# Performance work log

Measured on AMD Instinct MI355X. Metric: run time of the kernel, lower is better.

## Reference

```python
import jax, jax.numpy as jnp
import numpy as np

KS = 2            # kernel_size
NUM_SHARED = 3    # len(num_shared_channels)
NBR_PARAM = 3     # nbr_param_layers
COUT = 128        # num_shared_channels[-1] == num_inputs
NUM_INPUTS = 128
D_R = 320         # ts2vec_output_dims
GEN_LEN = NBR_PARAM * COUT * COUT * KS


def _causal_conv(x, w, b, d):
    # x: [N, Ci, T], w: [Co, Ci, K], b: [Co]; left-pad (K-1)*d == pad+chomp in torch
    N, Ci, T = x.shape
    K = w.shape[-1]
    pad = (K - 1) * d
    xp = jnp.pad(x, ((0, 0), (0, 0), (pad, 0)))
    out = jnp.zeros((N, w.shape[0], T), dtype=x.dtype)
    for k in range(K):  # K==2, tiny static loop
        out = out + jnp.einsum('oc,nct->not', w[:, :, k], xp[:, :, k * d:k * d + T])
    return out + b[None, :, None]


def _causal_conv_group(x, w, d):
    # groups=N conv with per-sample weights. x: [N, C, T], w: [N, Co, C, K], no bias
    N, C, T = x.shape
    K = w.shape[-1]
    pad = (K - 1) * d
    xp = jnp.pad(x, ((0, 0), (0, 0), (pad, 0)))
    out = jnp.zeros((N, w.shape[1], T), dtype=x.dtype)
    for k in range(K):
        out = out + jnp.einsum('noc,nct->not', w[..., k], xp[:, :, k * d:k * d + T])
    return out


def setup_inputs() -> dict:
    key = jax.random.key(0)
    ks = jax.random.split(key, 12)
    N, T = 16, 1024
    x = jax.random.normal(ks[0], (N, T, NUM_INPUTS), dtype=jnp.float32)
    r = jax.random.normal(ks[1], (N, D_R), dtype=jnp.float32)
    # shared TemporalBlock params (in==out==COUT, so no downsample conv)
    wscale = 1.0 / np.sqrt(COUT * KS)
    shared_w1 = wscale * jax.random.normal(ks[2], (NUM_SHARED, COUT, COUT, KS), dtype=jnp.float32)
    shared_b1 = 0.01 * jax.random.normal(ks[3], (NUM_SHARED, COUT), dtype=jnp.float32)
    shared_w2 = wscale * jax.random.normal(ks[4], (NUM_SHARED, COUT, COUT, KS), dtype=jnp.float32)
    shared_b2 = 0.01 * jax.random.normal(ks[5], (NUM_SHARED, COUT), dtype=jnp.float32)
    # hypernetwork (f_param_generator) + additive base weights (last_conv_layers)
    fparam_W = 0.01 * jax.random.normal(ks[6], (GEN_LEN, D_R), dtype=jnp.float32)
    fparam_b = 0.01 * jax.random.normal(ks[7], (GEN_LEN,), dtype=jnp.float32)
    last_bias = 0.001 * jax.random.normal(ks[8], (GEN_LEN,), dtype=jnp.float32) + 1.0 / (KS * COUT)
    # output head
    lin_W = (1.0 / np.sqrt(COUT)) * jax.random.normal(ks[9], (NUM_INPUTS, COUT), dtype=jnp.float32)
    lin_b = 0.01 * jax.random.normal(ks[10], (NUM_INPUTS,), dtype=jnp.float32)
    return {"x": x, "r": r, "f_out_same_in_size": 1,
            "shared_w1": shared_w1, "shared_b1": shared_b1,
            "shared_w2": shared_w2, "shared_b2": shared_b2,
            "fparam_W": fparam_W, "fparam_b": fparam_b, "last_bias": last_bias,
            "lin_W": lin_W, "lin_b": lin_b}


def reference(x, r, f_out_same_in_size, shared_w1, shared_b1, shared_w2, shared_b2,
              fparam_W, fparam_b, last_bias, lin_W, lin_b):
    N, T, _ = x.shape
    h = jnp.swapaxes(x, 1, 2)  # [N, C, T]
    # shared TemporalBlocks (dropout p=0 -> identity)
    for i in range(NUM_SHARED):
        d = 2 ** i
        res = h
        a = jax.nn.relu(_causal_conv(h, shared_w1[i], shared_b1[i], d))
        a = jax.nn.relu(_causal_conv(a, shared_w2[i], shared_b2[i], d))
        h = jax.nn.relu(a + res)
    # hypernet-generated per-sample grouped conv layers
    gen = r @ fparam_W.T + fparam_b + last_bias           # [N, GEN_LEN]
    allw = gen.reshape(NBR_PARAM, N, COUT, COUT, KS)      # same layout as torch .view
    for i in range(NBR_PARAM):
        d = 2 ** (NUM_SHARED + i)
        res = h
        c = _causal_conv_group(h, allw[i], d)
        h = jax.nn.relu(jax.nn.relu(c) + res)             # relu(dropout(relu(c)) + res), p=0
    out = jnp.einsum('nct,oc->nto', h, lin_W) + lin_b     # [N, T, NUM_INPUTS]
    if not f_out_same_in_size:
        out = out[:, -1, :]
    return out
```

## Files before the change

kernel.cpp:

```cpp
#include <hip/hip_runtime.h>

#define NB    16
#define TLEN  1024
#define CCH   128
#define DR    320
#define GENL  98304

typedef _Float16 h8 __attribute__((ext_vector_type(8)));
typedef _Float16 h4 __attribute__((ext_vector_type(4)));
typedef float    f4 __attribute__((ext_vector_type(4)));

__device__ __forceinline__ void gload16h(const _Float16* g, _Float16* l) {
  __builtin_amdgcn_global_load_lds(
      (const __attribute__((address_space(1))) void*)g,
      (__attribute__((address_space(3))) void*)l, 16, 0, 0);
}
__device__ __forceinline__ void gload16f(const float* g, float* l) {
  __builtin_amdgcn_global_load_lds(
      (const __attribute__((address_space(1))) void*)g,
      (__attribute__((address_space(3))) void*)l, 16, 0, 0);
}
__device__ __forceinline__ void gload4f(const float* g, float* l) {
  __builtin_amdgcn_global_load_lds(
      (const __attribute__((address_space(1))) void*)g,
      (__attribute__((address_space(3))) void*)l, 4, 0, 0);
}

__global__ __launch_bounds__(256) void k_cast(const float* __restrict__ x,
                                              _Float16* __restrict__ h) {
  int i = blockIdx.x * 256 + threadIdx.x;
  const float4* src = (const float4*)x + (size_t)i * 2;
  float4 a = src[0], b = src[1];
  h8 v;
  v[0] = (_Float16)a.x; v[1] = (_Float16)a.y; v[2] = (_Float16)a.z; v[3] = (_Float16)a.w;
  v[4] = (_Float16)b.x; v[5] = (_Float16)b.y; v[6] = (_Float16)b.z; v[7] = (_Float16)b.w;
  *(h8*)(h + (size_t)i * 8) = v;
}

__global__ __launch_bounds__(256) void k_prep_w(const float* __restrict__ w1,
                                                const float* __restrict__ w2,
                                                const float* __restrict__ linw,
                                                _Float16* __restrict__ Wsh,
                                                _Float16* __restrict__ linWh) {
  int idx = blockIdx.x * 256 + threadIdx.x;
  if (idx < 6 * 32768) {
    int c = idx & 127, k = (idx >> 7) & 1, o = (idx >> 8) & 127, i = idx >> 15;
    const float* src = (i < 3) ? (w1 + i * 32768) : (w2 + (i - 3) * 32768);
    Wsh[idx] = (_Float16)src[(o * 128 + c) * 2 + k];
  }
  if (idx < 16384) linWh[idx] = (_Float16)linw[idx];
}

__global__ __launch_bounds__(256) void k_gen3(const float* __restrict__ r,
                                              const float* __restrict__ fW,
                                              const float* __restrict__ fb,
                                              const float* __restrict__ lb,
                                              _Float16* __restrict__ wg) {
  __shared__ alignas(16) float rl[16 * DR];
  __shared__ alignas(16) float buf[2][32 * DR];
  __shared__ alignas(16) float csc[4][16][16];
  __shared__ float fbsc[32], lbsc[32];
  const int tid = threadIdx.x;
  const size_t rbase = (size_t)blockIdx.x * 384;

#pragma unroll
  for (int i = 0; i < 5; i++) {
    int f = tid + i * 256;
    gload16f(r + (size_t)f * 4, rl + (size_t)f * 4);
  }
  {
    const float* s0 = fW + rbase * DR;
#pragma unroll
    for (int i = 0; i < 10; i++) {
      int f = tid + i * 256;
      gload16f(s0 + (size_t)f * 4, (float*)buf[0] + (size_t)f * 4);
    }
    const float* s1 = fW + (rbase + 32) * DR;
#pragma unroll
    for (int i = 0; i < 10; i++) {
      int f = tid + i * 256;
      gload16f(s1 + (size_t)f * 4, (float*)buf[1] + (size_t)f * 4);
    }
  }
  asm volatile("s_waitcnt vmcnt(0) lgkmcnt(0)" ::: "memory");
  __builtin_amdgcn_s_barrier();
  __builtin_amdgcn_sched_barrier(0);

  const int l = tid & 63, w = tid >> 6;
  const int l15 = l & 15, lh = l >> 4;
  const int rt = w >> 1, kh = w & 1;

  h8 bfr[5];
#pragma unroll
  for (int cb = 0; cb < 5; cb++) {
    const float* p = &rl[l15 * DR + kh * 160 + cb * 32 + lh * 8];
    f4 x = *(const f4*)p, y = *(const f4*)(p + 4);
    h8 v;
    v[0] = (_Float16)x[0]; v[1] = (_Float16)x[1]; v[2] = (_Float16)x[2]; v[3] = (_Float16)x[3];
    v[4] = (_Float16)y[0]; v[5] = (_Float16)y[1]; v[6] = (_Float16)y[2]; v[7] = (_Float16)y[3];
    bfr[cb] = v;
  }

  for (int j = 0; j < 12; j++) {
    const float* bp = buf[j & 1];
    const int g32 = (int)rbase + j * 32;

    if (tid < 32) {
      gload4f(fb + g32 + tid, &fbsc[0]);
      gload4f(lb + g32 + tid, &lbsc[0]);
    }

    f4 acc = {0.f, 0.f, 0.f, 0.f};
    const float* arow = bp + (rt * 16 + l15) * DR + kh * 160 + lh * 8;
#pragma unroll
    for (int cb = 0; cb < 5; cb++) {
      f4 x = *(const f4*)(arow + cb * 32);
      f4 y = *(const f4*)(arow + cb * 32 + 4);
      h8 a;
      a[0] = (_Float16)x[0]; a[1] = (_Float16)x[1]; a[2] = (_Float16)x[2]; a[3] = (_Float16)x[3];
      a[4] = (_Float16)y[0]; a[5] = (_Float16)y[1]; a[6] = (_Float16)y[2]; a[7] = (_Float16)y[3];
      acc = __builtin_amdgcn_mfma_f32_16x16x32_f16(a, bfr[cb], acc, 0, 0, 0);
    }
#pragma unroll
    for (int rr = 0; rr < 4; rr++) csc[w][lh * 4 + rr][l15] = acc[rr];

    asm volatile("s_waitcnt vmcnt(0) lgkmcnt(0)" ::: "memory");
    __builtin_amdgcn_s_barrier();
    __builtin_amdgcn_sched_barrier(0);

    if (tid < 128) {
      int n = tid >> 3, k = (tid >> 2) & 1, cq = tid & 3;
      unsigned g = (unsigned)g32;
      unsigned G = g >> 15, o = (g >> 8) & 127u, c0 = (g & 255u) >> 1;
      h4 v;
#pragma unroll
      for (int i = 0; i < 4; i++) {
        int rl32 = (cq * 4 + i) * 2 + k;
        int hp = (rl32 >> 4) * 2, rr = rl32 & 15;
        float s = csc[hp][rr][n] + csc[hp + 1][rr][n] + fbsc[rl32] + lbsc[rl32];
        v[i] = (_Float16)s;
      }
      unsigned q = 3u * (unsigned)n + G;
      *(h4*)&wg[(((size_t)q * 128 + o) * 2 + k) * 128 + c0 + cq * 4] = v;
    }

    if (j + 2 < 12) {
      float* dst = (float*)buf[j & 1];
      const float* src = fW + (rbase + (size_t)(j + 2) * 32) * DR;
#pragma unroll
      for (int i = 0; i < 10; i++) {
        int f = tid + i * 256;
        gload16f(src + (size_t)f * 4, dst + (size_t)f * 4);
      }
    }

    asm volatile("s_waitcnt lgkmcnt(0)" ::: "memory");
    __builtin_amdgcn_s_barrier();
    __builtin_amdgcn_sched_barrier(0);
  }
}

template <int D>
__global__ __launch_bounds__(256) void k_pair(const _Float16* __restrict__ in,
                                              _Float16* __restrict__ out,
                                              const _Float16* __restrict__ w1p,
                                              const _Float16* __restrict__ w2p,
                                              const float* __restrict__ b1p,
                                              const float* __restrict__ b2p) {
  constexpr int HA = 16;
  constexpr int HI = HA + D;
  constexpr int RIN = 80 + D;
  __shared__ _Float16 hin_l[RIN * 128];
  __shared__ _Float16 a_l[80 * 128];

  const int tid = threadIdx.x;
  const int n = blockIdx.y, t0 = blockIdx.x * 64;
  const _Float16* inN = in + (size_t)n * (TLEN * CCH);

  if (blockIdx.x == 0) {
    for (int f = tid; f < HI * 16; f += 256)
      *(int4*)(hin_l + (size_t)f * 8) = make_int4(0, 0, 0, 0);
    for (int f = HI * 16 + tid; f < RIN * 16; f += 256) {
      int p = f >> 4, l16 = f & 15;
      int c8 = (l16 ^ (p & 15)) << 3;
      gload16h(inN + (t0 - HI + p) * 128 + c8, hin_l + f * 8);
    }
  } else {
    for (int f = tid; f < RIN * 16; f += 256) {
      int p = f >> 4, l16 = f & 15;
      int c8 = (l16 ^ (p & 15)) << 3;
      gload16h(inN + (t0 - HI + p) * 128 + c8, hin_l + f * 8);
    }
  }
  __syncthreads();

  const int l = tid & 63, w = tid >> 6;
  const int l15 = l & 15, lh = l >> 4;
  const int o0 = w * 32;

  f4 acc1[2][5] = {};
#pragma unroll
  for (int tap = 0; tap < 2; tap++) {
#pragma unroll
    for (int cb = 0; cb < 4; cb++) {
      const int c0 = cb * 32 + lh * 8;
      h8 a[2], bfr[5];
#pragma unroll
      for (int i2 = 0; i2 < 2; i2++) {
        int o = o0 + i2 * 16 + l15;
        a[i2] = *(const h8*)&w1p[(o * 2 + tap) * 128 + c0];
      }
#pragma unroll
      for (int jt = 0; jt < 5; jt++) {
        int p = jt * 16 + l15 + tap * D;
        int cs = c0 ^ ((p & 15) << 3);
        bfr[jt] = *(const h8*)&hin_l[p * 128 + cs];
      }
#pragma unroll
      for (int i2 = 0; i2 < 2; i2++)
#pragma unroll
        for (int jt = 0; jt < 5; jt++)
          acc1[i2][jt] = __builtin_amdgcn_mfma_f32_16x16x32_f16(
              a[i2], bfr[jt], acc1[i2][jt], 0, 0, 0);
    }
  }
#pragma unroll
  for (int i2 = 0; i2 < 2; i2++) {
    f4 bv = *(const f4*)&b1p[o0 + i2 * 16 + lh * 4];
    const int base8 = o0 + i2 * 16 + (lh >> 1) * 8;
    const int sub = (lh & 1) * 4;
#pragma unroll
    for (int jt = 0; jt < 5; jt++) {
      int p = jt * 16 + l15;
      h4 sv;
      if (blockIdx.x == 0 && jt == 0) {
        sv[0] = sv[1] = sv[2] = sv[3] = (_Float16)0.f;
      } else {
        f4 v = acc1[i2][jt];
#pragma unroll
        for (int rr = 0; rr < 4; rr++) sv[rr] = (_Float16)fmaxf(v[rr] + bv[rr], 0.f);
      }
      *(h4*)&a_l[p * 128 + (base8 ^ ((p & 15) << 3)) + sub] = sv;
    }
  }
  __syncthreads();

  f4 acc2[2][4] = {};
#pragma unroll
  for (int tap = 0; tap < 2; tap++) {
#pragma unroll
    for (int cb = 0; cb < 4; cb++) {
      const int c0 = cb * 32 + lh * 8;
      h8 a[2], bfr[4];
#pragma unroll
      for (int i2 = 0; i2 < 2; i2++) {
        int o = o0 + i2 * 16 + l15;
        a[i2] = *(const h8*)&w2p[(o * 2 + tap) * 128 + c0];
      }
#pragma unroll
      for (int jt = 0; jt < 4; jt++) {
        int pa = jt * 16 + l15 + (HA - D) + tap * D;
        int cs = c0 ^ ((pa & 15) << 3);
        bfr[jt] = *(const h8*)&a_l[pa * 128 + cs];
      }
#pragma unroll
      for (int i2 = 0; i2 < 2; i2++)
#pragma unroll
        for (int jt = 0; jt < 4; jt++)
          acc2[i2][jt] = __builtin_amdgcn_mfma_f32_16x16x32_f16(
              a[i2], bfr[jt], acc2[i2][jt], 0, 0, 0);
    }
  }

  _Float16* outN = out + (size_t)n * (TLEN * CCH);
#pragma unroll
  for (int i2 = 0; i2 < 2; i2++) {
    f4 bv = *(const f4*)&b2p[o0 + i2 * 16 + lh * 4];
    const int base8 = o0 + i2 * 16 + (lh >> 1) * 8;
    const int sub = (lh & 1) * 4;
#pragma unroll
    for (int jt = 0; jt < 4; jt++) {
      int t = t0 + jt * 16 + l15;
      int pr = jt * 16 + l15 + HA + D;
      h4 rv = *(const h4*)&hin_l[pr * 128 + (base8 ^ ((pr & 15) << 3)) + sub];
      f4 v = acc2[i2][jt];
      h4 sv;
#pragma unroll
      for (int rr = 0; rr < 4; rr++) {
        float z = fmaxf(v[rr] + bv[rr], 0.f);
        sv[rr] = (_Float16)fmaxf(z + (float)rv[rr], 0.f);
      }
      *(h4*)&outN[t * 128 + o0 + i2 * 16 + lh * 4] = sv;
    }
  }
}

template <int D>
__global__ __launch_bounds__(256) void k_gconv(const _Float16* __restrict__ in,
                                               _Float16* __restrict__ out,
                                               const _Float16* __restrict__ wBase) {
  __shared__ _Float16 Wl[256 * 128];
  __shared__ _Float16 hl[(64 + D) * 128];
  const int tid = threadIdx.x;
  const int n = blockIdx.y, t0 = blockIdx.x * 64;
  const _Float16* inN = in + (size_t)n * (TLEN * CCH);
  const _Float16* wp = wBase + (size_t)n * 32768;

  for (int f = tid; f < 4096; f += 256) {
    int row = f >> 4, l16 = f & 15;
    int c8 = (l16 ^ ((row >> 1) & 15)) << 3;
    gload16h(wp + row * 128 + c8, Wl + f * 8);
  }
  if (blockIdx.x == 0) {
    for (int f = tid; f < D * 16; f += 256)
      *(int4*)(hl + (size_t)f * 8) = make_int4(0, 0, 0, 0);
    for (int f = D * 16 + tid; f < (64 + D) * 16; f += 256) {
      int p = f >> 4, l16 = f & 15;
      int c8 = (l16 ^ (p & 15)) << 3;
      gload16h(inN + (t0 - D + p) * 128 + c8, hl + f * 8);
    }
  } else {
    for (int f = tid; f < (64 + D) * 16; f += 256) {
      int p = f >> 4, l16 = f & 15;
      int c8 = (l16 ^ (p & 15)) << 3;
      gload16h(inN + (t0 - D + p) * 128 + c8, hl + f * 8);
    }
  }
  __syncthreads();

  const int l = tid & 63, w = tid >> 6;
  const int l15 = l & 15, lh = l >> 4;
  const int o0 = w * 32;
  f4 acc[2][4] = {};

#pragma unroll
  for (int tap = 0; tap < 2; tap++) {
#pragma unroll
    for (int cb = 0; cb < 4; cb++) {
      const int c0 = cb * 32 + 8 * lh;
      h8 a[2], bfr[4];
#pragma unroll
      for (int i2 = 0; i2 < 2; i2++) {
        int o = o0 + i2 * 16 + l15;
        int cs = c0 ^ ((o & 15) << 3);
        a[i2] = *(const h8*)&Wl[(o * 2 + tap) * 128 + cs];
      }
#pragma unroll
      for (int jt = 0; jt < 4; jt++) {
        int p = jt * 16 + l15 + tap * D;
        int cs = c0 ^ ((p & 15) << 3);
        bfr[jt] = *(const h8*)&hl[p * 128 + cs];
      }
#pragma unroll
      for (int i2 = 0; i2 < 2; i2++)
#pragma unroll
        for (int jt = 0; jt < 4; jt++)
          acc[i2][jt] = __builtin_amdgcn_mfma_f32_16x16x32_f16(
              a[i2], bfr[jt], acc[i2][jt], 0, 0, 0);
    }
  }

  _Float16* outN = out + (size_t)n * (TLEN * CCH);
#pragma unroll
  for (int i2 = 0; i2 < 2; i2++) {
    const int base8 = o0 + i2 * 16 + (lh >> 1) * 8;
    const int sub = (lh & 1) * 4;
#pragma unroll
    for (int jt = 0; jt < 4; jt++) {
      int t = t0 + jt * 16 + l15;
      int pr = jt * 16 + l15 + D;
      h4 rv = *(const h4*)&hl[pr * 128 + (base8 ^ ((pr & 15) << 3)) + sub];
      f4 v = acc[i2][jt];
      h4 sv;
#pragma unroll
      for (int rr = 0; rr < 4; rr++) {
        float z = fmaxf(v[rr], 0.f);
        sv[rr] = (_Float16)fmaxf(z + (float)rv[rr], 0.f);
      }
      *(h4*)&outN[t * 128 + o0 + i2 * 16 + lh * 4] = sv;
    }
  }
}

__global__ __launch_bounds__(256) void k_glin(const _Float16* __restrict__ in,
                                              float* __restrict__ outp,
                                              const _Float16* __restrict__ wBase,
                                              const _Float16* __restrict__ linWh,
                                              const float* __restrict__ lbias) {
  constexpr int D = 32;
  __shared__ _Float16 Wl[256 * 128];
  __shared__ _Float16 hl[(64 + D) * 128];
  __shared__ _Float16 a_l[64 * 128];
  const int tid = threadIdx.x;
  const int n = blockIdx.y, t0 = blockIdx.x * 64;
  const _Float16* inN = in + (size_t)n * (TLEN * CCH);
  const _Float16* wp = wBase + (size_t)n * 32768;

  for (int f = tid; f < 4096; f += 256) {
    int row = f >> 4, l16 = f & 15;
    int c8 = (l16 ^ ((row >> 1) & 15)) << 3;
    gload16h(wp + row * 128 + c8, Wl + f * 8);
  }
  if (blockIdx.x == 0) {
    for (int f = tid; f < D * 16; f += 256)
      *(int4*)(hl + (size_t)f * 8) = make_int4(0, 0, 0, 0);
    for (int f = D * 16 + tid; f < (64 + D) * 16; f += 256) {
      int p = f >> 4, l16 = f & 15;
      int c8 = (l16 ^ (p & 15)) << 3;
      gload16h(inN + (t0 - D + p) * 128 + c8, hl + f * 8);
    }
  } else {
    for (int f = tid; f < (64 + D) * 16; f += 256) {
      int p = f >> 4, l16 = f & 15;
      int c8 = (l16 ^ (p & 15)) << 3;
      gload16h(inN + (t0 - D + p) * 128 + c8, hl + f * 8);
    }
  }
  __syncthreads();

  const int l = tid & 63, w = tid >> 6;
  const int l15 = l & 15, lh = l >> 4;
  const int o0 = w * 32;
  f4 acc[2][4] = {};

#pragma unroll
  for (int tap = 0; tap < 2; tap++) {
#pragma unroll
    for (int cb = 0; cb < 4; cb++) {
      const int c0 = cb * 32 + 8 * lh;
      h8 a[2], bfr[4];
#pragma unroll
      for (int i2 = 0; i2 < 2; i2++) {
        int o = o0 + i2 * 16 + l15;
        int cs = c0 ^ ((o & 15) << 3);
        a[i2] = *(const h8*)&Wl[(o * 2 + tap) * 128 + cs];
      }
#pragma unroll
      for (int jt = 0; jt < 4; jt++) {
        int p = jt * 16 + l15 + tap * D;
        int cs = c0 ^ ((p & 15) << 3);
        bfr[jt] = *(const h8*)&hl[p * 128 + cs];
      }
#pragma unroll
      for (int i2 = 0; i2 < 2; i2++)
#pragma unroll
        for (int jt = 0; jt < 4; jt++)
          acc[i2][jt] = __builtin_amdgcn_mfma_f32_16x16x32_f16(
              a[i2], bfr[jt], acc[i2][jt], 0, 0, 0);
    }
  }

#pragma unroll
  for (int i2 = 0; i2 < 2; i2++) {
    const int base8 = o0 + i2 * 16 + (lh >> 1) * 8;
    const int sub = (lh & 1) * 4;
#pragma unroll
    for (int jt = 0; jt < 4; jt++) {
      int p = jt * 16 + l15;
      int pr = p + D;
      h4 rv = *(const h4*)&hl[pr * 128 + (base8 ^ ((pr & 15) << 3)) + sub];
      f4 v = acc[i2][jt];
      h4 sv;
#pragma unroll
      for (int rr = 0; rr < 4; rr++) {
        float z = fmaxf(v[rr], 0.f);
        sv[rr] = (_Float16)fmaxf(z + (float)rv[rr], 0.f);
      }
      *(h4*)&a_l[p * 128 + (base8 ^ (l15 << 3)) + sub] = sv;
    }
  }
  __syncthreads();

  f4 acc3[2][4] = {};
#pragma unroll
  for (int cb = 0; cb < 4; cb++) {
    const int c0 = cb * 32 + lh * 8;
    h8 a[2], bfr[4];
#pragma unroll
    for (int i2 = 0; i2 < 2; i2++) {
      int o = o0 + i2 * 16 + l15;
      a[i2] = *(const h8*)&linWh[o * 128 + c0];
    }
#pragma unroll
    for (int jt = 0; jt < 4; jt++) {
      int p = jt * 16 + l15;
      int cs = c0 ^ ((p & 15) << 3);
      bfr[jt] = *(const h8*)&a_l[p * 128 + cs];
    }
#pragma unroll
    for (int i2 = 0; i2 < 2; i2++)
#pragma unroll
      for (int jt = 0; jt < 4; jt++)
        acc3[i2][jt] = __builtin_amdgcn_mfma_f32_16x16x32_f16(
            a[i2], bfr[jt], acc3[i2][jt], 0, 0, 0);
  }

#pragma unroll
  for (int i2 = 0; i2 < 2; i2++) {
    int o = o0 + i2 * 16 + lh * 4;
    f4 bv = *(const f4*)&lbias[o];
#pragma unroll
    for (int jt = 0; jt < 4; jt++) {
      int t = t0 + jt * 16 + l15;
      f4 v = acc3[i2][jt];
      float4 sv = make_float4(v[0] + bv[0], v[1] + bv[1], v[2] + bv[2], v[3] + bv[3]);
      *(float4*)&outp[((size_t)n * TLEN + t) * CCH + o] = sv;
    }
  }
}

extern "C" void kernel_launch(void* const* d_in, const int* in_sizes, int n_in,
                              void* d_out, int out_size, void* d_ws, size_t ws_size,
                              hipStream_t stream) {
  const float* x  = (const float*)d_in[0];
  const float* r  = (const float*)d_in[1];
  const float* w1 = (const float*)d_in[3];
  const float* b1 = (const float*)d_in[4];
  const float* w2 = (const float*)d_in[5];
  const float* b2 = (const float*)d_in[6];
  const float* fW = (const float*)d_in[7];
  const float* fb = (const float*)d_in[8];
  const float* lb = (const float*)d_in[9];
  const float* lw = (const float*)d_in[10];
  const float* lbias = (const float*)d_in[11];
  float* out = (float*)d_out;

  _Float16* h0    = (_Float16*)d_ws;
  _Float16* h1    = h0 + 2097152;
  _Float16* Wsh   = h1 + 2097152;
  _Float16* linWh = Wsh + 393216;
  _Float16* Wg    = linWh + 16384;

  k_cast<<<1024, 256, 0, stream>>>(x, h0);
  k_prep_w<<<768, 256, 0, stream>>>(w1, w2, lw, Wsh, linWh);
  k_gen3<<<256, 256, 0, stream>>>(r, fW, fb, lb, Wg);

  const dim3 cg(16, 16);
  k_pair<1><<<cg, 256, 0, stream>>>(h0, h1, Wsh + 0 * 32768, Wsh + 3 * 32768,
                                    b1 + 0 * 128, b2 + 0 * 128);
  k_pair<2><<<cg, 256, 0, stream>>>(h1, h0, Wsh + 1 * 32768, Wsh + 4 * 32768,
                                    b1 + 1 * 128, b2 + 1 * 128);
  k_pair<4><<<cg, 256, 0, stream>>>(h0, h1, Wsh + 2 * 32768, Wsh + 5 * 32768,
                                    b1 + 2 * 128, b2 + 2 * 128);
  k_gconv<8> <<<cg, 256, 0, stream>>>(h1, h0, Wg + (size_t)0 * 16 * 32768);
  k_gconv<16><<<cg, 256, 0, stream>>>(h0, h1, Wg + (size_t)1 * 16 * 32768);
  k_glin<<<cg, 256, 0, stream>>>(h1, out, Wg + (size_t)2 * 16 * 32768, linWh, lbias);
}
```

Baseline: 81.69 us.

## Merge prep kernels and triple-buffer the hypernetwork weight generator

Folds the input cast, the shared-weight conversion and a precomputed fb+lb sum into one init kernel, removing a launch. The generator kernel now keeps three fW tiles in flight instead of two and uses partial vmcnt waits so loads overlap the MFMA work. It reads r directly into registers rather than staging it in LDS, and spreads the epilogue writes over all 256 threads. The precise vmcnt counts are fragile and must exactly match the number of outstanding loads.

```diff
diff --git a/kernel.cpp b/kernel.cpp
--- a/kernel.cpp
+++ b/kernel.cpp
@@ -4,10 +4,10 @@
 #define TLEN  1024
 #define CCH   128
 #define DR    320
-#define GENL  98304
 
 typedef _Float16 h8 __attribute__((ext_vector_type(8)));
 typedef _Float16 h4 __attribute__((ext_vector_type(4)));
+typedef _Float16 h2 __attribute__((ext_vector_type(2)));
 typedef float    f4 __attribute__((ext_vector_type(4)));
 
 __device__ __forceinline__ void gload16h(const _Float16* g, _Float16* l) {
@@ -20,96 +20,83 @@
       (const __attribute__((address_space(1))) void*)g,
       (__attribute__((address_space(3))) void*)l, 16, 0, 0);
 }
-__device__ __forceinline__ void gload4f(const float* g, float* l) {
-  __builtin_amdgcn_global_load_lds(
-      (const __attribute__((address_space(1))) void*)g,
-      (__attribute__((address_space(3))) void*)l, 4, 0, 0);
-}
-
-__global__ __launch_bounds__(256) void k_cast(const float* __restrict__ x,
-                                              _Float16* __restrict__ h) {
+
+__global__ __launch_bounds__(256) void k_init(const float* __restrict__ x,
+                                              const float* __restrict__ w1,
+                                              const float* __restrict__ w2,
+                                              const float* __restrict__ linw,
+                                              const float* __restrict__ fb,
+                                              const float* __restrict__ lb,
+                                              _Float16* __restrict__ h0,
+                                              _Float16* __restrict__ Wsh,
+                                              _Float16* __restrict__ linWh,
+                                              float* __restrict__ fblb2) {
   int i = blockIdx.x * 256 + threadIdx.x;
   const float4* src = (const float4*)x + (size_t)i * 2;
   float4 a = src[0], b = src[1];
   h8 v;
   v[0] = (_Float16)a.x; v[1] = (_Float16)a.y; v[2] = (_Float16)a.z; v[3] = (_Float16)a.w;
   v[4] = (_Float16)b.x; v[5] = (_Float16)b.y; v[6] = (_Float16)b.z; v[7] = (_Float16)b.w;
-  *(h8*)(h + (size_t)i * 8) = v;
-}
-
-__global__ __launch_bounds__(256) void k_prep_w(const float* __restrict__ w1,
-                                                const float* __restrict__ w2,
-                                                const float* __restrict__ linw,
-                                                _Float16* __restrict__ Wsh,
-                                                _Float16* __restrict__ linWh) {
-  int idx = blockIdx.x * 256 + threadIdx.x;
-  if (idx < 6 * 32768) {
-    int c = idx & 127, k = (idx >> 7) & 1, o = (idx >> 8) & 127, i = idx >> 15;
-    const float* src = (i < 3) ? (w1 + i * 32768) : (w2 + (i - 3) * 32768);
-    Wsh[idx] = (_Float16)src[(o * 128 + c) * 2 + k];
-  }
-  if (idx < 16384) linWh[idx] = (_Float16)linw[idx];
-}
-
-__global__ __launch_bounds__(256) void k_gen3(const float* __restrict__ r,
+  *(h8*)(h0 + (size_t)i * 8) = v;
+
+  if (i < 6 * 32768) {
+    int c = i & 127, k = (i >> 7) & 1, o = (i >> 8) & 127, i3 = i >> 15;
+    const float* srcw = (i3 < 3) ? (w1 + i3 * 32768) : (w2 + (i3 - 3) * 32768);
+    Wsh[i] = (_Float16)srcw[(o * 128 + c) * 2 + k];
+  }
+  if (i < 16384) linWh[i] = (_Float16)linw[i];
+  if (i < 98304) fblb2[i] = fb[i] + lb[i];
+}
+
+__global__ __launch_bounds__(256) void k_gen4(const float* __restrict__ r,
                                               const float* __restrict__ fW,
-                                              const float* __restrict__ fb,
-                                              const float* __restrict__ lb,
+                                              const float* __restrict__ fblb2,
                                               _Float16* __restrict__ wg) {
-  __shared__ alignas(16) float rl[16 * DR];
-  __shared__ alignas(16) float buf[2][32 * DR];
+  __shared__ alignas(16) float buf[3][32 * DR];
   __shared__ alignas(16) float csc[4][16][16];
-  __shared__ float fbsc[32], lbsc[32];
+  __shared__ alignas(16) float fbl[384];
   const int tid = threadIdx.x;
   const size_t rbase = (size_t)blockIdx.x * 384;
-
-#pragma unroll
-  for (int i = 0; i < 5; i++) {
-    int f = tid + i * 256;
-    gload16f(r + (size_t)f * 4, rl + (size_t)f * 4);
-  }
-  {
-    const float* s0 = fW + rbase * DR;
-#pragma unroll
-    for (int i = 0; i < 10; i++) {
-      int f = tid + i * 256;
-      gload16f(s0 + (size_t)f * 4, (float*)buf[0] + (size_t)f * 4);
-    }
-    const float* s1 = fW + (rbase + 32) * DR;
-#pragma unroll
-    for (int i = 0; i < 10; i++) {
-      int f = tid + i * 256;
-      gload16f(s1 + (size_t)f * 4, (float*)buf[1] + (size_t)f * 4);
-    }
-  }
-  asm volatile("s_waitcnt vmcnt(0) lgkmcnt(0)" ::: "memory");
-  __builtin_amdgcn_s_barrier();
-  __builtin_amdgcn_sched_barrier(0);
 
   const int l = tid & 63, w = tid >> 6;
   const int l15 = l & 15, lh = l >> 4;
   const int rt = w >> 1, kh = w & 1;
 
+  f4 rx[5], ry[5];
+  const float* rp = r + l15 * DR + kh * 160 + lh * 8;
+#pragma unroll
+  for (int cb = 0; cb < 5; cb++) {
+    rx[cb] = *(const f4*)(rp + cb * 32);
+    ry[cb] = *(const f4*)(rp + cb * 32 + 4);
+  }
+  if (tid < 96) gload16f(fblb2 + rbase + tid * 4, fbl + tid * 4);
+#pragma unroll
+  for (int t = 0; t < 3; t++) {
+    const float* s = fW + (rbase + (size_t)t * 32) * DR;
+#pragma unroll
+    for (int i = 0; i < 10; i++) {
+      int f = tid + i * 256;
+      gload16f(s + (size_t)f * 4, (float*)buf[t] + (size_t)f * 4);
+    }
+  }
   h8 bfr[5];
 #pragma unroll
   for (int cb = 0; cb < 5; cb++) {
-    const float* p = &rl[l15 * DR + kh * 160 + cb * 32 + lh * 8];
-    f4 x = *(const f4*)p, y = *(const f4*)(p + 4);
     h8 v;
-    v[0] = (_Float16)x[0]; v[1] = (_Float16)x[1]; v[2] = (_Float16)x[2]; v[3] = (_Float16)x[3];
-    v[4] = (_Float16)y[0]; v[5] = (_Float16)y[1]; v[6] = (_Float16)y[2]; v[7] = (_Float16)y[3];
+    v[0] = (_Float16)rx[cb][0]; v[1] = (_Float16)rx[cb][1];
+    v[2] = (_Float16)rx[cb][2]; v[3] = (_Float16)rx[cb][3];
+    v[4] = (_Float16)ry[cb][0]; v[5] = (_Float16)ry[cb][1];
+    v[6] = (_Float16)ry[cb][2]; v[7] = (_Float16)ry[cb][3];
     bfr[cb] = v;
   }
+  asm volatile("s_waitcnt vmcnt(20) lgkmcnt(0)" ::: "memory");
+  __builtin_amdgcn_s_barrier();
+  __builtin_amdgcn_sched_barrier(0);
+
+  const int rn = tid >> 4, rk = (tid >> 3) & 1, rcq = tid & 7;
 
   for (int j = 0; j < 12; j++) {
-    const float* bp = buf[j & 1];
-    const int g32 = (int)rbase + j * 32;
-
-    if (tid < 32) {
-      gload4f(fb + g32 + tid, &fbsc[0]);
-      gload4f(lb + g32 + tid, &lbsc[0]);
-    }
-
+    const float* bp = (const float*)buf[j % 3];
     f4 acc = {0.f, 0.f, 0.f, 0.f};
     const float* arow = bp + (rt * 16 + l15) * DR + kh * 160 + lh * 8;
 #pragma unroll
@@ -117,44 +104,50 @@
       f4 x = *(const f4*)(arow + cb * 32);
       f4 y = *(const f4*)(arow + cb * 32 + 4);
       h8 a;
-      a[0] = (_Float16)x[0]; a[1] = (_Float16)x[1]; a[2] = (_Float16)x[2]; a[3] = (_Float16)x[3];
-      a[4] = (_Float16)y[0]; a[5] = (_Float16)y[1]; a[6] = (_Float16)y[2]; a[7] = (_Float16)y[3];
+      a[0] = (_Float16)x[0]; a[1] = (_Float16)x[1];
+      a[2] = (_Float16)x[2]; a[3] = (_Float16)x[3];
+      a[4] = (_Float16)y[0]; a[5] = (_Float16)y[1];
+      a[6] = (_Float16)y[2]; a[7] = (_Float16)y[3];
       acc = __builtin_amdgcn_mfma_f32_16x16x32_f16(a, bfr[cb], acc, 0, 0, 0);
     }
 #pragma unroll
     for (int rr = 0; rr < 4; rr++) csc[w][lh * 4 + rr][l15] = acc[rr];
 
-    asm volatile("s_waitcnt vmcnt(0) lgkmcnt(0)" ::: "memory");
+    asm volatile("s_waitcnt lgkmcnt(0)" ::: "memory");
     __builtin_amdgcn_s_barrier();
     __builtin_amdgcn_sched_barrier(0);
 
-    if (tid < 128) {
-      int n = tid >> 3, k = (tid >> 2) & 1, cq = tid & 3;
-      unsigned g = (unsigned)g32;
-      unsigned G = g >> 15, o = (g >> 8) & 127u, c0 = (g & 255u) >> 1;
-      h4 v;
-#pragma unroll
-      for (int i = 0; i < 4; i++) {
-        int rl32 = (cq * 4 + i) * 2 + k;
-        int hp = (rl32 >> 4) * 2, rr = rl32 & 15;
-        float s = csc[hp][rr][n] + csc[hp + 1][rr][n] + fbsc[rl32] + lbsc[rl32];
-        v[i] = (_Float16)s;
-      }
-      unsigned q = 3u * (unsigned)n + G;
-      *(h4*)&wg[(((size_t)q * 128 + o) * 2 + k) * 128 + c0 + cq * 4] = v;
-    }
-
-    if (j + 2 < 12) {
-      float* dst = (float*)buf[j & 1];
-      const float* src = fW + (rbase + (size_t)(j + 2) * 32) * DR;
+    {
+      const unsigned g32 = (unsigned)(rbase + (size_t)j * 32);
+      const unsigned G = g32 >> 15, o = (g32 >> 8) & 127u, c0 = (g32 & 255u) >> 1;
+      h2 v2;
+#pragma unroll
+      for (int i = 0; i < 2; i++) {
+        int rl32 = (rcq * 2 + i) * 2 + rk;
+        int hp = (rl32 >> 4) * 2, rr2 = rl32 & 15;
+        float s = csc[hp][rr2][rn] + csc[hp + 1][rr2][rn] + fbl[j * 32 + rl32];
+        v2[i] = (_Float16)s;
+      }
+      unsigned q = 3u * (unsigned)rn + G;
+      *(h2*)&wg[(((size_t)q * 128 + o) * 2 + rk) * 128 + c0 + rcq * 2] = v2;
+    }
+
+    if (j <= 8) {
+      float* dstb = (float*)buf[j % 3];
+      const float* src = fW + (rbase + (size_t)(j + 3) * 32) * DR;
 #pragma unroll
       for (int i = 0; i < 10; i++) {
         int f = tid + i * 256;
-        gload16f(src + (size_t)f * 4, dst + (size_t)f * 4);
-      }
-    }
-
-    asm volatile("s_waitcnt lgkmcnt(0)" ::: "memory");
+        gload16f(src + (size_t)f * 4, dstb + (size_t)f * 4);
+      }
+    }
+
+    if (j < 10)
+      asm volatile("s_waitcnt vmcnt(11) lgkmcnt(0)" ::: "memory");
+    else if (j == 10)
+      asm volatile("s_waitcnt vmcnt(2) lgkmcnt(0)" ::: "memory");
+    else
+      asm volatile("s_waitcnt vmcnt(0) lgkmcnt(0)" ::: "memory");
     __builtin_amdgcn_s_barrier();
     __builtin_amdgcn_sched_barrier(0);
   }
@@ -530,19 +523,19 @@
   _Float16* Wsh   = h1 + 2097152;
   _Float16* linWh = Wsh + 393216;
   _Float16* Wg    = linWh + 16384;
-
-  k_cast<<<1024, 256, 0, stream>>>(x, h0);
-  k_prep_w<<<768, 256, 0, stream>>>(w1, w2, lw, Wsh, linWh);
-  k_gen3<<<256, 256, 0, stream>>>(r, fW, fb, lb, Wg);
+  float*    fblb2 = (float*)(Wg + 1572864);
+
+  k_init<<<1024, 256, 0, stream>>>(x, w1, w2, lw, fb, lb, h0, Wsh, linWh, fblb2);
+  k_gen4<<<256, 256, 0, stream>>>(r, fW, fblb2, Wg);
 
   const dim3 cg(16, 16);
   k_pair<1><<<cg, 256, 0, stream>>>(h0, h1, Wsh + 0 * 32768, Wsh + 3 * 32768,
-                                    b1 + 0 * 128, b2 + 0 * 128);
+                                    b1, b2);
   k_pair<2><<<cg, 256, 0, stream>>>(h1, h0, Wsh + 1 * 32768, Wsh + 4 * 32768,
-                                    b1 + 1 * 128, b2 + 1 * 128);
+                                    b1 + 128, b2 + 128);
   k_pair<4><<<cg, 256, 0, stream>>>(h0, h1, Wsh + 2 * 32768, Wsh + 5 * 32768,
-                                    b1 + 2 * 128, b2 + 2 * 128);
-  k_gconv<8> <<<cg, 256, 0, stream>>>(h1, h0, Wg + (size_t)0 * 16 * 32768);
-  k_gconv<16><<<cg, 256, 0, stream>>>(h0, h1, Wg + (size_t)1 * 16 * 32768);
-  k_glin<<<cg, 256, 0, stream>>>(h1, out, Wg + (size_t)2 * 16 * 32768, linWh, lbias);
-}
+                                    b1 + 256, b2 + 256);
+  k_gconv<8> <<<cg, 256, 0, stream>>>(h1, h0, Wg);
+  k_gconv<16><<<cg, 256, 0, stream>>>(h0, h1, Wg + 524288);
+  k_glin<<<cg, 256, 0, stream>>>(h1, out, Wg + 1048576, linWh, lbias);
+}
```

Measured after the change: 82.63 us. Within noise of the previous version (+1.1%).
